# Optimization experiments

Measured on AMD Instinct MI355X. Metric: run time of the kernel, lower is better.

Reference implementation:

```python
import jax, jax.numpy as jnp
import numpy as np
from jax import lax

N_HEADS = 8
D_K = 64
D_V = 64
TEMP = float(np.sqrt(D_K))  # MixtureOfSoftMax temperature = d_k ** 0.5


def avg_pool_3x3_s2_same(x):
    """TF-style AveragePooling2D(pool=3, stride=2, padding='same'), NHWC.
    TF excludes padded elements from the average (divide by valid count)."""
    sums = lax.reduce_window(x, 0.0, lax.add, (1, 3, 3, 1), (1, 2, 2, 1), 'SAME')
    ones = jnp.ones(x.shape[:3] + (1,), x.dtype)
    cnt = lax.reduce_window(ones, 0.0, lax.add, (1, 3, 3, 1), (1, 2, 2, 1), 'SAME')
    return sums / cnt


def conv1x1(x, w, b):
    # 1x1 conv == per-pixel channel matmul
    return jnp.einsum('bhwc,cd->bhwd', x, w) + b


def setup_inputs() -> dict:
    key = jax.random.key(0)
    ks = jax.random.split(key, 6)
    C = 512
    s1 = float(np.sqrt(2.0 / (C + D_K)))  # init_weight1 std
    s3 = float(np.sqrt(2.0 / (C + D_V)))  # init_weight3 std
    return {
        'x':   jax.random.normal(ks[0], (4, 64, 64, C), jnp.float32),
        'w_q': jax.random.normal(ks[1], (C, N_HEADS * D_K), jnp.float32) * s1,
        'b_q': jnp.zeros((N_HEADS * D_K,), jnp.float32),
        'w_k': jax.random.normal(ks[2], (C, N_HEADS * D_K), jnp.float32) * s1,
        'b_k': jnp.zeros((N_HEADS * D_K,), jnp.float32),
        'w_v': jax.random.normal(ks[3], (C, N_HEADS * D_V), jnp.float32) * s3,
        'b_v': jnp.zeros((N_HEADS * D_V,), jnp.float32),
        'w_o': jax.random.normal(ks[4], (N_HEADS * D_V, C), jnp.float32) * 0.02,
        'b_o': jnp.zeros((C,), jnp.float32),
    }


def reference(x, w_q, b_q, w_k, b_k, w_v, b_v, w_o, b_o):
    BS, H, W, C = x.shape
    residual = x
    # Q from full-res x; K, V from 3x3/s2 average-pooled x (pooling=True)
    qt = conv1x1(x, w_q, b_q).reshape(BS * N_HEADS, H * W, -1)          # (B*h, N, d_k)
    xp = avg_pool_3x3_s2_same(x)                                         # (BS, H/2, W/2, C)
    kt = conv1x1(xp, w_k, b_k).reshape(BS * N_HEADS, H * W // 4, -1)     # (B*h, N/4, d_k)
    vt = conv1x1(xp, w_v, b_v).reshape(BS * N_HEADS, H * W // 4, -1)     # (B*h, N/4, d_v)
    # MixtureOfSoftMaxACF with n_mix=1: scaled dot-product softmax attention
    attn = jnp.einsum('bnd,bmd->bnm', qt, kt) / TEMP                     # (B*h, N, N/4)
    attn = jax.nn.softmax(attn, axis=-1)                                 # dropout=identity (inference)
    out = jnp.einsum('bnm,bmd->bnd', attn, vt)                           # (B*h, N, d_v)
    out = out.reshape(BS, H, W, -1)
    out = conv1x1(out, w_o, b_o)                                         # conv1x1_bn_relu (Conv2D only in call)
    return out + residual                                                # concat=False -> Add
```

## Files before the change

kernel.cpp:

```cpp
#include <hip/hip_runtime.h>
#include <hip/hip_bf16.h>
#include <math.h>

typedef short bf16x8 __attribute__((ext_vector_type(8)));
typedef float f32x4 __attribute__((ext_vector_type(4)));
typedef unsigned short u16;

__device__ inline float b2f(u16 h) {
    unsigned int u = ((unsigned int)h) << 16;
    float f;
    __builtin_memcpy(&f, &u, 4);
    return f;
}

__device__ inline u16 f2b(float f) {
    unsigned int u;
    __builtin_memcpy(&u, &f, 4);
    unsigned int lsb = (u >> 16) & 1u;
    u += 0x7fffu + lsb;
    return (u16)(u >> 16);
}

__device__ __forceinline__ void gl2lds16(const u16* g, u16* l) {
    __builtin_amdgcn_global_load_lds(
        (const __attribute__((address_space(1))) unsigned int*)g,
        (__attribute__((address_space(3))) unsigned int*)l,
        16, 0, 0);
}

#define PITCH 72

#define QSCALE 0.18033688011112042f

__global__ __launch_bounds__(256) void cvt_kernel(const float* __restrict__ x,
                                                  u16* __restrict__ xb) {
    int idx = blockIdx.x * 256 + threadIdx.x;
    float4 v = ((const float4*)x)[idx];
    ushort4 o;
    o.x = f2b(v.x); o.y = f2b(v.y); o.z = f2b(v.z); o.w = f2b(v.w);
    ((ushort4*)xb)[idx] = o;
}

__global__ __launch_bounds__(256) void wtrans_kernel(const float* __restrict__ w0,
                                                     const float* __restrict__ w1,
                                                     const float* __restrict__ w2,
                                                     const float* __restrict__ w3,
                                                     u16* __restrict__ wt) {
    const float* W = blockIdx.z == 0 ? w0 : blockIdx.z == 1 ? w1
                   : blockIdx.z == 2 ? w2 : w3;
    u16* WT = wt + (size_t)blockIdx.z * 262144;
    __shared__ u16 T[64 * PITCH];
    int tid = threadIdx.x;
    int nB = blockIdx.x * 64, kB = blockIdx.y * 64;
#pragma unroll
    for (int t = 0; t < 4; ++t) {
        int e = tid + t * 256;
        int r = e >> 4, c4 = (e & 15) * 4;
        float4 v = *(const float4*)(&W[(size_t)(kB + r) * 512 + nB + c4]);
        u16* dst = &T[r * PITCH + c4];
        dst[0] = f2b(v.x); dst[1] = f2b(v.y); dst[2] = f2b(v.z); dst[3] = f2b(v.w);
    }
    __syncthreads();
    int n = tid & 63, kg = tid >> 6;
#pragma unroll
    for (int p = 0; p < 2; ++p) {
        int k0 = (kg + p * 4) * 8;
        u16 tmp[8];
#pragma unroll
        for (int i = 0; i < 8; ++i) tmp[i] = T[(k0 + i) * PITCH + n];
        *(int4*)(&WT[(size_t)(nB + n) * 512 + kB + k0]) = *(int4*)tmp;
    }
}

__global__ __launch_bounds__(256) void pool_kernel(const u16* __restrict__ xb,
                                                   u16* __restrict__ xp) {
    int idx = blockIdx.x * 256 + threadIdx.x;
    int c8 = idx & 63;
    int j = (idx >> 6) & 31;
    int i = (idx >> 11) & 31;
    int b = idx >> 16;
    int r0 = 2 * i, c0 = 2 * j;
    int rmax = min(r0 + 3, 64), cmax = min(c0 + 3, 64);
    float acc[8] = {};
    for (int r = r0; r < rmax; ++r)
        for (int cc = c0; cc < cmax; ++cc) {
            bf16x8 v = *(const bf16x8*)(
                &xb[(size_t)((((b << 6) + r) << 6) + cc) * 512 + c8 * 8]);
#pragma unroll
            for (int t = 0; t < 8; ++t) acc[t] += b2f(((const u16*)&v)[t]);
        }
    float inv = 1.f / (float)((rmax - r0) * (cmax - c0));
    u16 o[8];
#pragma unroll
    for (int t = 0; t < 8; ++t) o[t] = f2b(acc[t] * inv);
    *(int4*)(&xp[(size_t)idx * 8]) = *(int4*)o;
}

template <int OM>
__global__ __launch_bounds__(256, 4) void gemm_bf16(const u16* __restrict__ A,
                                                    const u16* __restrict__ WT,
                                                    const float* __restrict__ bias,
                                                    const float* __restrict__ bias2res,
                                                    void* __restrict__ Cv,
                                                    void* __restrict__ Cv2,
                                                    float oscale) {
    __shared__ __align__(16) u16 At[64 * 64];
    __shared__ __align__(16) u16 Bt[128 * 64];
    int tid = threadIdx.x, lane = tid & 63, wave = tid >> 6;
    int q = lane >> 4, l16 = lane & 15;
    int wm = wave & 1, wn = wave >> 1;
    int bid = blockIdx.y * gridDim.x + blockIdx.x;
    int nBlk = bid / gridDim.y;
    int mBlk = bid - nBlk * gridDim.y;
    int nBase = nBlk * 128, mBase = mBlk * 64;
    f32x4 acc[2][4] = {};

    for (int kk = 0; kk < 512; kk += 64) {
        __syncthreads();
#pragma unroll
        for (int t = 0; t < 2; ++t) {
            int c = tid + t * 256;
            int m = c >> 3, kc = (c & 7) ^ (m & 7);
            gl2lds16(&A[(size_t)(mBase + m) * 512 + kk + kc * 8], &At[c * 8]);
        }
#pragma unroll
        for (int t = 0; t < 4; ++t) {
            int c = tid + t * 256;
            int m = c >> 3, kc = (c & 7) ^ (m & 7);
            gl2lds16(&WT[(size_t)(nBase + m) * 512 + kk + kc * 8], &Bt[c * 8]);
        }
        __syncthreads();
#pragma unroll
        for (int ds = 0; ds < 2; ++ds) {
            bf16x8 a[2], b[4];
#pragma unroll
            for (int i = 0; i < 2; ++i) {
                int ma = wm * 32 + i * 16 + l16;
                a[i] = *(bf16x8*)(&At[ma * 64 + ((((ds << 2) + q) ^ (ma & 7)) << 3)]);
            }
#pragma unroll
            for (int j = 0; j < 4; ++j) {
                int nb = wn * 64 + j * 16 + l16;
                b[j] = *(bf16x8*)(&Bt[nb * 64 + ((((ds << 2) + q) ^ (nb & 7)) << 3)]);
            }
#pragma unroll
            for (int i = 0; i < 2; ++i)
#pragma unroll
                for (int j = 0; j < 4; ++j)
                    acc[i][j] = __builtin_amdgcn_mfma_f32_16x16x32_bf16(a[i], b[j], acc[i][j], 0, 0, 0);
        }
    }

    bool isK = (OM != 3) || (nBase < 512);
#pragma unroll
    for (int j = 0; j < 4; ++j) {
        int col = nBase + wn * 64 + j * 16 + l16;
        float bv;
        if constexpr (OM == 3) bv = isK ? bias[col] : bias2res[col - 512];
        else bv = bias[col];
#pragma unroll
        for (int i = 0; i < 2; ++i) {
#pragma unroll
            for (int r = 0; r < 4; ++r) {
                int row = mBase + wm * 32 + i * 16 + q * 4 + r;
                float v = acc[i][j][r] + bv;
                if constexpr (OM == 1) {
                    v += bias2res[(size_t)row * 512 + col];
                    ((float*)Cv)[(size_t)row * 512 + col] = v;
                } else if constexpr (OM == 0) {
                    ((u16*)Cv)[(size_t)row * 512 + col] = f2b(v * oscale);
                } else {
                    if (isK) {
                        ((u16*)Cv)[(size_t)row * 512 + col] = f2b(v);
                    } else {
                        int colv = col - 512;
                        int g = row >> 7, m2 = ((row & 127) << 3) + (colv >> 6), d = colv & 63;
                        ((u16*)Cv2)[(size_t)((g << 6) + d) * 1024 + m2] = f2b(v);
                    }
                }
            }
        }
    }
}

__global__ __launch_bounds__(256, 4) void attn_kernel(const u16* __restrict__ Q,
                                                      const u16* __restrict__ K,
                                                      const u16* __restrict__ VT_g,
                                                      u16* __restrict__ O) {
    int g = blockIdx.x;
    int qtile = blockIdx.y;
    const u16* Qg = Q + (size_t)g * 262144;
    const u16* Kg = K + (size_t)g * 65536;
    const u16* Vt = VT_g + (size_t)g * 65536;
    u16* Og = O + (size_t)g * 262144;

    __shared__ __align__(16) u16 Kt[128 * 64];
    __shared__ __align__(16) u16 VTs[64 * 128];
    __shared__ __align__(16) u16 Pt[64 * 64];

    int tid = threadIdx.x, lane = tid & 63, wave = tid >> 6;
    int q = lane >> 4, l16 = lane & 15;
    int n0 = qtile * 128;
    int pkey = (l16 & 7) << 2;
    int prow = (wave * 16 + l16) * 32;
    int* Pt32 = (int*)Pt;

    bf16x8 qf[2][2];
#pragma unroll
    for (int s = 0; s < 2; ++s)
#pragma unroll
        for (int ds = 0; ds < 2; ++ds)
            qf[s][ds] = *(const bf16x8*)(
                &Qg[(size_t)(n0 + s * 64 + wave * 16 + l16) * 64 + ds * 32 + q * 8]);

    f32x4 oacc[2][4] = {};
    float rsum[2] = {0.f, 0.f};

    for (int kb = 0; kb < 8; ++kb) {
        __syncthreads();
#pragma unroll
        for (int t = 0; t < 4; ++t) {
            int c = wave * 64 + lane + t * 256;
            {
                int m = c >> 3, kc = (c & 7) ^ (m & 7);
                gl2lds16(&Kg[(size_t)(kb * 128 + m) * 64 + kc * 8], &Kt[c * 8]);
            }
            {
                int d = c >> 4, mc = (c & 15) ^ (d & 15);
                gl2lds16(&Vt[(size_t)d * 1024 + kb * 128 + mc * 8], &VTs[c * 8]);
            }
        }
        __syncthreads();

#pragma unroll
        for (int h = 0; h < 2; ++h) {
#pragma unroll
            for (int s = 0; s < 2; ++s) {
#pragma unroll
                for (int cb = 0; cb < 4; ++cb) {
                    int m = h * 64 + cb * 16 + l16;
                    bf16x8 kf0 = *(bf16x8*)(&Kt[m * 64 + ((q ^ (m & 7)) << 3)]);
                    bf16x8 kf1 = *(bf16x8*)(&Kt[m * 64 + (((4 + q) ^ (m & 7)) << 3)]);
                    f32x4 z = {};
                    __builtin_amdgcn_s_setprio(1);
                    z = __builtin_amdgcn_mfma_f32_16x16x32_bf16(kf0, qf[s][0], z, 0, 0, 0);
                    z = __builtin_amdgcn_mfma_f32_16x16x32_bf16(kf1, qf[s][1], z, 0, 0, 0);
                    __builtin_amdgcn_s_setprio(0);
                    float p0 = __builtin_amdgcn_exp2f(z[0]);
                    float p1 = __builtin_amdgcn_exp2f(z[1]);
                    float p2 = __builtin_amdgcn_exp2f(z[2]);
                    float p3 = __builtin_amdgcn_exp2f(z[3]);
                    rsum[s] += (p0 + p1) + (p2 + p3);
                    unsigned w0, w1;
                    asm("v_cvt_pk_bf16_f32 %0, %1, %2" : "=v"(w0) : "v"(p0), "v"(p1));
                    asm("v_cvt_pk_bf16_f32 %0, %1, %2" : "=v"(w1) : "v"(p2), "v"(p3));
                    int2 w;
                    w.x = (int)w0;
                    w.y = (int)w1;
                    int pd = (cb * 8 + q * 2) ^ pkey;
                    *(int2*)(&Pt32[prow + pd]) = w;
                }
#pragma unroll
                for (int ds = 0; ds < 2; ++ds) {
                    int pd = (ds * 16 + q * 4) ^ pkey;
                    bf16x8 ap = *(bf16x8*)(&Pt32[prow + pd]);
                    __builtin_amdgcn_s_setprio(1);
#pragma unroll
                    for (int db = 0; db < 4; ++db) {
                        int dd = db * 16 + l16;
                        int jj = h * 8 + ds * 4 + q;
                        bf16x8 vb = *(bf16x8*)(&VTs[dd * 128 + ((jj ^ (dd & 15)) << 3)]);
                        oacc[s][db] = __builtin_amdgcn_mfma_f32_16x16x32_bf16(ap, vb, oacc[s][db], 0, 0, 0);
                    }
                    __builtin_amdgcn_s_setprio(0);
                }
            }
        }
    }

#pragma unroll
    for (int s = 0; s < 2; ++s) {
        float v = rsum[s];
        v += __shfl_xor(v, 16, 64);
        v += __shfl_xor(v, 32, 64);
        rsum[s] = v;
    }
    float inv[2][4];
#pragma unroll
    for (int s = 0; s < 2; ++s)
#pragma unroll
        for (int r = 0; r < 4; ++r)
            inv[s][r] = 1.f / __shfl(rsum[s], q * 4 + r, 64);
#pragma unroll
    for (int s = 0; s < 2; ++s)
#pragma unroll
        for (int db = 0; db < 4; ++db)
#pragma unroll
            for (int r = 0; r < 4; ++r) {
                int row = n0 + s * 64 + wave * 16 + q * 4 + r;
                Og[(size_t)row * 64 + db * 16 + l16] = f2b(oacc[s][db][r] * inv[s][r]);
            }
}

extern "C" void kernel_launch(void* const* d_in, const int* in_sizes, int n_in,
                              void* d_out, int out_size, void* d_ws, size_t ws_size,
                              hipStream_t stream) {
    const float* x   = (const float*)d_in[0];
    const float* w_q = (const float*)d_in[1];
    const float* b_q = (const float*)d_in[2];
    const float* w_k = (const float*)d_in[3];
    const float* b_k = (const float*)d_in[4];
    const float* w_v = (const float*)d_in[5];
    const float* b_v = (const float*)d_in[6];
    const float* w_o = (const float*)d_in[7];
    const float* b_o = (const float*)d_in[8];
    float* out = (float*)d_out;

    char* ws = (char*)d_ws;
    u16* xb  = (u16*)(ws);
    u16* xp  = (u16*)(ws + (16ull << 20));
    u16* Qw  = (u16*)(ws + (20ull << 20));
    u16* Kw  = (u16*)(ws + (36ull << 20));
    u16* VwT = (u16*)(ws + (40ull << 20));
    u16* wT  = (u16*)(ws + (44ull << 20));
    u16* Ow  = xb;

    cvt_kernel<<<8192, 256, 0, stream>>>(x, xb);
    wtrans_kernel<<<dim3(8, 8, 4), 256, 0, stream>>>(w_q, w_k, w_v, w_o, wT);
    pool_kernel<<<1024, 256, 0, stream>>>(xb, xp);
    gemm_bf16<0><<<dim3(4, 256), 256, 0, stream>>>(xb, wT, b_q, nullptr, Qw, nullptr, QSCALE);
    gemm_bf16<3><<<dim3(8, 64), 256, 0, stream>>>(xp, wT + 262144, b_k, b_v, Kw, VwT, 1.0f);
    attn_kernel<<<dim3(32, 32), 256, 0, stream>>>(Qw, Kw, VwT, Ow);
    gemm_bf16<1><<<dim3(4, 256), 256, 0, stream>>>(Ow, wT + 786432, b_o, x, out, nullptr, 1.0f);
}
```

Measured before the change: 200.5 us.

## Merge prologue kernels and retile K/V GEMM for more blocks

Combines the x conversion and weight transposition into one launch, and runs the Q projection GEMM alongside the average pooling in a single launch using block-index dispatch. Cuts launches from seven to five. The K/V GEMM moves to 64-wide N tiles with one M sub-tile per wave, doubling its block count to 1024 for better occupancy on a small problem. Costs are fewer MFMAs per LDS load in the KV GEMM and mixed-work blocks that sit at the GEMM's resource limits.

```diff
diff --git a/kernel.cpp b/kernel.cpp
--- a/kernel.cpp
+++ b/kernel.cpp
@@ -32,26 +32,28 @@
 
 #define QSCALE 0.18033688011112042f
 
-__global__ __launch_bounds__(256) void cvt_kernel(const float* __restrict__ x,
-                                                  u16* __restrict__ xb) {
-    int idx = blockIdx.x * 256 + threadIdx.x;
-    float4 v = ((const float4*)x)[idx];
-    ushort4 o;
-    o.x = f2b(v.x); o.y = f2b(v.y); o.z = f2b(v.z); o.w = f2b(v.w);
-    ((ushort4*)xb)[idx] = o;
-}
-
-__global__ __launch_bounds__(256) void wtrans_kernel(const float* __restrict__ w0,
-                                                     const float* __restrict__ w1,
-                                                     const float* __restrict__ w2,
-                                                     const float* __restrict__ w3,
-                                                     u16* __restrict__ wt) {
-    const float* W = blockIdx.z == 0 ? w0 : blockIdx.z == 1 ? w1
-                   : blockIdx.z == 2 ? w2 : w3;
-    u16* WT = wt + (size_t)blockIdx.z * 262144;
+__global__ __launch_bounds__(256) void cvtw_kernel(const float* __restrict__ x,
+                                                   u16* __restrict__ xb,
+                                                   const float* __restrict__ w0,
+                                                   const float* __restrict__ w1,
+                                                   const float* __restrict__ w2,
+                                                   const float* __restrict__ w3,
+                                                   u16* __restrict__ wt) {
     __shared__ u16 T[64 * PITCH];
     int tid = threadIdx.x;
-    int nB = blockIdx.x * 64, kB = blockIdx.y * 64;
+    if (blockIdx.x < 8192) {
+        int idx = blockIdx.x * 256 + tid;
+        float4 v = ((const float4*)x)[idx];
+        ushort4 o;
+        o.x = f2b(v.x); o.y = f2b(v.y); o.z = f2b(v.z); o.w = f2b(v.w);
+        ((ushort4*)xb)[idx] = o;
+        return;
+    }
+    int t5 = blockIdx.x - 8192;
+    int bx = t5 & 7, by = (t5 >> 3) & 7, bz = t5 >> 6;
+    const float* W = bz == 0 ? w0 : bz == 1 ? w1 : bz == 2 ? w2 : w3;
+    u16* WT = wt + (size_t)bz * 262144;
+    int nB = bx * 64, kB = by * 64;
 #pragma unroll
     for (int t = 0; t < 4; ++t) {
         int e = tid + t * 256;
@@ -72,9 +74,8 @@
     }
 }
 
-__global__ __launch_bounds__(256) void pool_kernel(const u16* __restrict__ xb,
-                                                   u16* __restrict__ xp) {
-    int idx = blockIdx.x * 256 + threadIdx.x;
+__device__ __forceinline__ void pool_body(int idx, const u16* __restrict__ xb,
+                                          u16* __restrict__ xp) {
     int c8 = idx & 63;
     int j = (idx >> 6) & 31;
     int i = (idx >> 11) & 31;
@@ -96,24 +97,26 @@
     *(int4*)(&xp[(size_t)idx * 8]) = *(int4*)o;
 }
 
-template <int OM>
-__global__ __launch_bounds__(256, 4) void gemm_bf16(const u16* __restrict__ A,
-                                                    const u16* __restrict__ WT,
-                                                    const float* __restrict__ bias,
-                                                    const float* __restrict__ bias2res,
-                                                    void* __restrict__ Cv,
-                                                    void* __restrict__ Cv2,
-                                                    float oscale) {
-    __shared__ __align__(16) u16 At[64 * 64];
-    __shared__ __align__(16) u16 Bt[128 * 64];
+template <int OM, int BN, int GY>
+__device__ __forceinline__ void gemm_body(int bid,
+                                          const u16* __restrict__ A,
+                                          const u16* __restrict__ WT,
+                                          const float* __restrict__ bias,
+                                          const float* __restrict__ bias2res,
+                                          void* __restrict__ Cv,
+                                          void* __restrict__ Cv2,
+                                          float oscale,
+                                          u16* At, u16* Bt) {
     int tid = threadIdx.x, lane = tid & 63, wave = tid >> 6;
     int q = lane >> 4, l16 = lane & 15;
-    int wm = wave & 1, wn = wave >> 1;
-    int bid = blockIdx.y * gridDim.x + blockIdx.x;
-    int nBlk = bid / gridDim.y;
-    int mBlk = bid - nBlk * gridDim.y;
-    int nBase = nBlk * 128, mBase = mBlk * 64;
-    f32x4 acc[2][4] = {};
+    constexpr int MI = (BN == 128) ? 2 : 1;
+    int wm, wn;
+    if constexpr (BN == 128) { wm = wave & 1; wn = wave >> 1; }
+    else                     { wm = wave;     wn = 0; }
+    int nBlk = bid / GY;
+    int mBlk = bid - nBlk * GY;
+    int nBase = nBlk * BN, mBase = mBlk * 64;
+    f32x4 acc[MI][4] = {};
 
     for (int kk = 0; kk < 512; kk += 64) {
         __syncthreads();
@@ -124,7 +127,7 @@
             gl2lds16(&A[(size_t)(mBase + m) * 512 + kk + kc * 8], &At[c * 8]);
         }
 #pragma unroll
-        for (int t = 0; t < 4; ++t) {
+        for (int t = 0; t < BN / 32; ++t) {
             int c = tid + t * 256;
             int m = c >> 3, kc = (c & 7) ^ (m & 7);
             gl2lds16(&WT[(size_t)(nBase + m) * 512 + kk + kc * 8], &Bt[c * 8]);
@@ -132,10 +135,10 @@
         __syncthreads();
 #pragma unroll
         for (int ds = 0; ds < 2; ++ds) {
-            bf16x8 a[2], b[4];
-#pragma unroll
-            for (int i = 0; i < 2; ++i) {
-                int ma = wm * 32 + i * 16 + l16;
+            bf16x8 a[MI], b[4];
+#pragma unroll
+            for (int i = 0; i < MI; ++i) {
+                int ma = (BN == 128 ? wm * 32 : wm * 16) + i * 16 + l16;
                 a[i] = *(bf16x8*)(&At[ma * 64 + ((((ds << 2) + q) ^ (ma & 7)) << 3)]);
             }
 #pragma unroll
@@ -144,7 +147,7 @@
                 b[j] = *(bf16x8*)(&Bt[nb * 64 + ((((ds << 2) + q) ^ (nb & 7)) << 3)]);
             }
 #pragma unroll
-            for (int i = 0; i < 2; ++i)
+            for (int i = 0; i < MI; ++i)
 #pragma unroll
                 for (int j = 0; j < 4; ++j)
                     acc[i][j] = __builtin_amdgcn_mfma_f32_16x16x32_bf16(a[i], b[j], acc[i][j], 0, 0, 0);
@@ -159,10 +162,10 @@
         if constexpr (OM == 3) bv = isK ? bias[col] : bias2res[col - 512];
         else bv = bias[col];
 #pragma unroll
-        for (int i = 0; i < 2; ++i) {
+        for (int i = 0; i < MI; ++i) {
 #pragma unroll
             for (int r = 0; r < 4; ++r) {
-                int row = mBase + wm * 32 + i * 16 + q * 4 + r;
+                int row = mBase + (BN == 128 ? wm * 32 : wm * 16) + i * 16 + q * 4 + r;
                 float v = acc[i][j][r] + bv;
                 if constexpr (OM == 1) {
                     v += bias2res[(size_t)row * 512 + col];
@@ -181,6 +184,42 @@
             }
         }
     }
+}
+
+__global__ __launch_bounds__(256, 4) void qpool_kernel(const u16* __restrict__ xb,
+                                                       const u16* __restrict__ wTq,
+                                                       const float* __restrict__ b_q,
+                                                       u16* __restrict__ Qw,
+                                                       u16* __restrict__ xp) {
+    __shared__ __align__(16) u16 At[64 * 64];
+    __shared__ __align__(16) u16 Bt[128 * 64];
+    int gid = blockIdx.x;
+    if (gid < 1024) {
+        gemm_body<0, 128, 256>(gid, xb, wTq, b_q, nullptr, Qw, nullptr, QSCALE, At, Bt);
+    } else {
+        pool_body((gid - 1024) * 256 + threadIdx.x, xb, xp);
+    }
+}
+
+__global__ __launch_bounds__(256, 4) void gemm_kv_kernel(const u16* __restrict__ xp,
+                                                         const u16* __restrict__ wTkv,
+                                                         const float* __restrict__ b_k,
+                                                         const float* __restrict__ b_v,
+                                                         u16* __restrict__ Kw,
+                                                         u16* __restrict__ VwT) {
+    __shared__ __align__(16) u16 At[64 * 64];
+    __shared__ __align__(16) u16 Bt[64 * 64];
+    gemm_body<3, 64, 64>(blockIdx.x, xp, wTkv, b_k, b_v, Kw, VwT, 1.0f, At, Bt);
+}
+
+__global__ __launch_bounds__(256, 4) void gemm_o_kernel(const u16* __restrict__ Ow,
+                                                        const u16* __restrict__ wTo,
+                                                        const float* __restrict__ b_o,
+                                                        const float* __restrict__ xres,
+                                                        float* __restrict__ out) {
+    __shared__ __align__(16) u16 At[64 * 64];
+    __shared__ __align__(16) u16 Bt[128 * 64];
+    gemm_body<1, 128, 256>(blockIdx.x, Ow, wTo, b_o, xres, out, nullptr, 1.0f, At, Bt);
 }
 
 __global__ __launch_bounds__(256, 4) void attn_kernel(const u16* __restrict__ Q,
@@ -325,11 +364,9 @@
     u16* wT  = (u16*)(ws + (44ull << 20));
     u16* Ow  = xb;
 
-    cvt_kernel<<<8192, 256, 0, stream>>>(x, xb);
-    wtrans_kernel<<<dim3(8, 8, 4), 256, 0, stream>>>(w_q, w_k, w_v, w_o, wT);
-    pool_kernel<<<1024, 256, 0, stream>>>(xb, xp);
-    gemm_bf16<0><<<dim3(4, 256), 256, 0, stream>>>(xb, wT, b_q, nullptr, Qw, nullptr, QSCALE);
-    gemm_bf16<3><<<dim3(8, 64), 256, 0, stream>>>(xp, wT + 262144, b_k, b_v, Kw, VwT, 1.0f);
+    cvtw_kernel<<<8448, 256, 0, stream>>>(x, xb, w_q, w_k, w_v, w_o, wT);
+    qpool_kernel<<<2048, 256, 0, stream>>>(xb, wT, b_q, Qw, xp);
+    gemm_kv_kernel<<<1024, 256, 0, stream>>>(xp, wT + 262144, b_k, b_v, Kw, VwT);
     attn_kernel<<<dim3(32, 32), 256, 0, stream>>>(Qw, Kw, VwT, Ow);
-    gemm_bf16<1><<<dim3(4, 256), 256, 0, stream>>>(Ow, wT + 786432, b_o, x, out, nullptr, 1.0f);
-}
+    gemm_o_kernel<<<1024, 256, 0, stream>>>(Ow, wT + 786432, b_o, x, out);
+}
```

Measured after the change: 196.8 us. Within noise of the previous version (-1.9%).
